# Performance work log

Measured on AMD Instinct MI355X. Metric: run time of the kernel, lower is better.

Reference implementation:

```python
import jax, jax.numpy as jnp
import numpy as np

B, N, I, H, O, E, HD = 4, 2048, 32, 64, 32, 2, 2  # batch, nodes, in_dim, hidden, out, edgetypes, heads
D1 = H * HD * E  # layer-1 filter input dim (concat of all heads/edgetypes from layer 0)


def setup_inputs() -> dict:
    key = jax.random.key(0)
    ks = jax.random.split(key, 20)
    s = 0.1
    return {
        "nodes": jax.random.normal(ks[0], (B, N, I), jnp.float32),
        "edges": jax.random.normal(ks[1], (B, N, N, E), jnp.float32),
        "W_emb": jax.random.normal(ks[2], (I, H), jnp.float32) * s,
        "b_emb": jnp.zeros((H,), jnp.float32),
        "Wf0": jax.random.normal(ks[3], (E, HD, H, H), jnp.float32) * s,
        "w1_0": jax.random.normal(ks[4], (E, HD, H), jnp.float32) * s,
        "b1_0": jnp.zeros((E, HD), jnp.float32),
        "w2_0": jax.random.normal(ks[5], (E, HD, H), jnp.float32) * s,
        "b2_0": jnp.zeros((E, HD), jnp.float32),
        "bias0": jax.random.normal(ks[6], (HD, H), jnp.float32) * s,  # state_bias aliased across edgetypes (list-mult bug)
        "Wf1": jax.random.normal(ks[7], (E, HD, D1, H), jnp.float32) * s,
        "w1_1": jax.random.normal(ks[8], (E, HD, H), jnp.float32) * s,
        "b1_1": jnp.zeros((E, HD), jnp.float32),
        "w2_1": jax.random.normal(ks[9], (E, HD, H), jnp.float32) * s,
        "b2_1": jnp.zeros((E, HD), jnp.float32),
        "bias1": jax.random.normal(ks[10], (HD, H), jnp.float32) * s,
        "W_out": jax.random.normal(ks[11], (H, O), jnp.float32) * s,
        "b_out": jnp.zeros((O,), jnp.float32),
    }


def _gat_layer(state, Wf, w1, b1, w2, b2, bias, edges_t, last):
    # state: (B,N,Din); Wf: (E,HD,Din,H); edges_t: (E,B,N,N)
    Wh = jnp.einsum('bnd,ehdk->ehbnk', state, Wf)                     # (E,HD,B,N,H)
    a1 = jnp.einsum('ehbnk,ehk->ehbn', Wh, w1) + b1[:, :, None, None]
    a2 = jnp.einsum('ehbnk,ehk->ehbn', Wh, w2) + b2[:, :, None, None]
    logits = jax.nn.leaky_relu(a1[..., :, None] + a2[..., None, :], 0.2) + edges_t[:, None]
    att = jax.nn.softmax(logits, axis=-2)                             # torch softmax dim=1 (over rows)
    msg = jnp.einsum('ehbik,ehbkd->ehbid', att, Wh) + bias[None, :, None, None, :]
    if last:
        return jnp.mean(jax.nn.elu(msg), axis=(0, 1))                 # (B,N,H)
    # concat in (edgetype-major, head-minor) order, matching the python loops
    return jnp.transpose(msg, (2, 3, 0, 1, 4)).reshape(msg.shape[2], msg.shape[3], -1)


def reference(nodes, edges, W_emb, b_emb, Wf0, w1_0, b1_0, w2_0, b2_0, bias0,
              Wf1, w1_1, b1_1, w2_1, b2_1, bias1, W_out, b_out):
    edges_t = jnp.transpose(edges, (3, 0, 1, 2))                      # (E,B,N,N)
    state = nodes @ W_emb + b_emb                                     # embedding
    state = _gat_layer(state, Wf0, w1_0, b1_0, w2_0, b2_0, bias0, edges_t, last=False)
    state = _gat_layer(state, Wf1, w1_1, b1_1, w2_1, b2_1, bias1, edges_t, last=True)
    out = state @ W_out + b_out                                       # (B,N,O)
    return jnp.mean(out, axis=1)                                      # graph-level output (B,O)
```

## Files before the change

### kernel.cpp

```cpp
#include <hip/hip_runtime.h>
#include <hip/hip_bf16.h>


constexpr int B_  = 4;
constexpr int N_  = 2048;
constexpr int I_  = 32;
constexpr int H_  = 64;
constexpr int O_  = 32;
constexpr int EH_ = 4;
constexpr int D1_ = 256;
constexpr int BN_ = B_ * N_;
constexpr int NC_ = 64;
constexpr int CH_ = N_ / NC_;
constexpr int TI_ = 16;
constexpr int TK_ = 32;
constexpr int NKT_ = N_ / TK_;

typedef __bf16 bf16x8 __attribute__((ext_vector_type(8)));
typedef float floatx4 __attribute__((ext_vector_type(4)));

constexpr float L2E_ = 1.4426950408889634f;

__device__ __forceinline__ unsigned short f2b(float f) {
    unsigned int u = __float_as_uint(f);
    return (unsigned short)((u + 0x7fffu + ((u >> 16) & 1u)) >> 16);
}

__device__ __forceinline__ float fexp2(float x) {
#if __has_builtin(__builtin_amdgcn_exp2f)
    return __builtin_amdgcn_exp2f(x);
#else
    return __expf(x * 0.6931471805599453f);
#endif
}

__global__ __launch_bounds__(256) void prep_kernel(
        const float* __restrict__ nodes, const float* __restrict__ W_emb,
        const float* __restrict__ b_emb, const float* __restrict__ Wf0,
        const float* __restrict__ Wf1, unsigned short* __restrict__ state0B,
        unsigned short* __restrict__ WfB0, unsigned short* __restrict__ WfB1) {
    int blk = blockIdx.x;
    int t = threadIdx.x;
    __shared__ float sn[4][I_];
    if (blk < 2048) {
        int r = t >> 6, h = t & 63;
        if (t < 4 * I_) {
            int rr = t / I_, ii = t % I_;
            sn[rr][ii] = nodes[(size_t)(blk * 4 + rr) * I_ + ii];
        }
        __syncthreads();
        float acc = b_emb[h];
        #pragma unroll
        for (int i = 0; i < I_; ++i) acc += sn[r][i] * W_emb[i * H_ + h];
        state0B[(size_t)(blk * 4 + r) * H_ + h] = f2b(acc);
    } else if (blk < 2048 + 64) {
        int o = (blk - 2048) * 256 + t;
        int k = o & 63, n = (o >> 6) & 63, c = o >> 12;
        WfB0[o] = f2b(Wf0[((size_t)c * 64 + k) * 64 + n]);
    } else {
        int o = (blk - 2112) * 256 + t;
        int k = o & 255, n = (o >> 8) & 63, c = o >> 14;
        WfB1[o] = f2b(Wf1[((size_t)c * 256 + k) * 64 + n]);
    }
}

template <int DIN>
__global__ __launch_bounds__(256) void wh_a_mfma_kernel(
        const unsigned short* __restrict__ stateB, const unsigned short* __restrict__ WfB,
        const float* __restrict__ w1, const float* __restrict__ b1,
        const float* __restrict__ w2, const float* __restrict__ b2,
        unsigned short* __restrict__ WhB, float* __restrict__ a1,
        float* __restrict__ a2) {
    int t = threadIdx.x;
    int lane = t & 63, wv = t >> 6;
    int col = lane & 15, qd = lane >> 4;
    int bn0 = blockIdx.x * TI_;
    int b = bn0 >> 11;

    floatx4 acc[4] = {{0,0,0,0},{0,0,0,0},{0,0,0,0},{0,0,0,0}};
    const unsigned short* __restrict__ ap = stateB + (size_t)(bn0 + col) * DIN + qd * 8;
    const unsigned short* __restrict__ bp = WfB + ((size_t)(wv * 64 + col) * DIN + qd * 8);
    #pragma unroll
    for (int k0 = 0; k0 < DIN; k0 += 32) {
        bf16x8 af = *(const bf16x8*)(ap + k0);
        #pragma unroll
        for (int nt = 0; nt < 4; ++nt) {
            bf16x8 bf = *(const bf16x8*)(bp + (size_t)nt * 16 * DIN + k0);
            acc[nt] = __builtin_amdgcn_mfma_f32_16x16x32_bf16(af, bf, acc[nt], 0, 0, 0);
        }
    }
    int nb = ((bn0 & 2047) >> 3) + (qd >> 1);
    #pragma unroll
    for (int nt = 0; nt < 4; ++nt) {
        unsigned int lo = (unsigned int)f2b(acc[nt][0]) | ((unsigned int)f2b(acc[nt][1]) << 16);
        unsigned int hi = (unsigned int)f2b(acc[nt][2]) | ((unsigned int)f2b(acc[nt][3]) << 16);
        uint2 v = make_uint2(lo, hi);
        *(uint2*)(WhB + ((((size_t)(wv * B_ + b) * 256 + nb) * 64 + nt * 16 + col) * 8
                         + (qd & 1) * 4)) = v;
    }
    float p1[4] = {}, p2[4] = {};
    #pragma unroll
    for (int nt = 0; nt < 4; ++nt) {
        float w1n = w1[wv * H_ + nt * 16 + col];
        float w2n = w2[wv * H_ + nt * 16 + col];
        #pragma unroll
        for (int r = 0; r < 4; ++r) {
            p1[r] += acc[nt][r] * w1n;
            p2[r] += acc[nt][r] * w2n;
        }
    }
    #pragma unroll
    for (int m = 1; m < 16; m <<= 1)
        #pragma unroll
        for (int r = 0; r < 4; ++r) {
            p1[r] += __shfl_xor(p1[r], m, 64);
            p2[r] += __shfl_xor(p2[r], m, 64);
        }
    if (col == 0) {
        float b1c = b1[wv], b2c = b2[wv];
        #pragma unroll
        for (int r = 0; r < 4; ++r) {
            a1[(size_t)wv * BN_ + bn0 + qd * 4 + r] = (p1[r] + b1c) * L2E_;
            a2[(size_t)wv * BN_ + bn0 + qd * 4 + r] = (p2[r] + b2c) * L2E_;
        }
    }
}

__global__ __launch_bounds__(256) void stats_kernel(
        const float* __restrict__ edges, const float* __restrict__ a1,
        const float* __restrict__ a2, float* __restrict__ ps) {
    int blk = blockIdx.x;
    int jt = blk & 3;
    int ic = (blk >> 2) & (NC_ - 1);
    int b  = blk >> 8;
    int t = threadIdx.x;
    int j0 = jt * 512 + t * 2;
    __shared__ float sa1[EH_][CH_];
    if (t < EH_ * CH_) {
        int cc = t >> 5, ii = t & 31;
        sa1[cc][ii] = a1[(size_t)cc * BN_ + b * N_ + ic * CH_ + ii];
    }
    __syncthreads();
    float a2x[EH_], a2y[EH_], s0[EH_], s1[EH_];
    #pragma unroll
    for (int cc = 0; cc < EH_; ++cc) {
        float2 av = *(const float2*)(a2 + (size_t)cc * BN_ + b * N_ + j0);
        a2x[cc] = av.x; a2y[cc] = av.y;
        s0[cc] = 0.f; s1[cc] = 0.f;
    }
    const float4* __restrict__ ep =
        (const float4*)edges + (((size_t)(b * N_ + ic * CH_) * N_ + j0) >> 1);
    #pragma unroll 4
    for (int ii = 0; ii < CH_; ++ii) {
        float4 u = ep[(size_t)ii * (N_ >> 1)];
        #pragma unroll
        for (int cc = 0; cc < EH_; ++cc) {
            float base = sa1[cc][ii];
            float xa = base + a2x[cc];
            float xb = base + a2y[cc];
            float la = fmaxf(xa, 0.2f * xa);
            float lb = fmaxf(xb, 0.2f * xb);
            float ea = (cc < 2) ? u.x : u.y;
            float eb = (cc < 2) ? u.z : u.w;
            s0[cc] += fexp2(fmaf(ea, L2E_, la));
            s1[cc] += fexp2(fmaf(eb, L2E_, lb));
        }
    }
    #pragma unroll
    for (int cc = 0; cc < EH_; ++cc)
        *(float2*)&ps[((size_t)ic * EH_ + cc) * BN_ + b * N_ + j0] =
            make_float2(s0[cc], s1[cc]);
}

__global__ __launch_bounds__(256) void scale_kernel(
        const float* __restrict__ ps, unsigned short* __restrict__ WhB) {
    int t = threadIdx.x;
    int m0 = blockIdx.x * 256;
    int cb = m0 >> 14;
    int c = cb >> 2, b = cb & 3;
    int k0 = ((m0 >> 6) & 255) * 8;
    __shared__ float sD[32];
    if (t < 32) {
        float S = 0.f;
        const float* pp = ps + (size_t)c * BN_ + b * N_ + k0 + t;
        #pragma unroll 8
        for (int ic = 0; ic < NC_; ++ic) S += pp[(size_t)ic * EH_ * BN_];
        sD[t] = 1.f / S;
    }
    __syncthreads();
    unsigned short* wp = WhB + (size_t)(m0 + t) * 8;
    uint4 w = *(const uint4*)wp;
    int nbo = (t >> 6) * 8;
    unsigned int words[4] = {w.x, w.y, w.z, w.w};
    #pragma unroll
    for (int q = 0; q < 4; ++q) {
        float lo = __uint_as_float((words[q] & 0xffffu) << 16) * sD[nbo + 2 * q];
        float hi = __uint_as_float(words[q] & 0xffff0000u) * sD[nbo + 2 * q + 1];
        words[q] = (unsigned)f2b(lo) | ((unsigned)f2b(hi) << 16);
    }
    *(uint4*)wp = make_uint4(words[0], words[1], words[2], words[3]);
}

template <int LAST>
__global__ __launch_bounds__(512, 8) void mac_kernel(
        const float* __restrict__ edges, const float* __restrict__ a1,
        const float* __restrict__ a2s, const unsigned short* __restrict__ WhB,
        const float* __restrict__ bias, void* __restrict__ outv) {
    int t = threadIdx.x;
    int blk = blockIdx.x;
    int cp = blk & 1;
    int g  = blk >> 1;
    int b  = g >> 7;
    int i0 = (g & 127) * TI_;
    int lane = t & 63, wv = t >> 6;
    int kq = wv >> 1;
    int cl = wv & 1;
    int c  = cp * 2 + cl;
    int col = lane & 15;
    int qd  = lane >> 4;

    __shared__ float sa2[2][N_];
    __shared__ float sA[2][TI_][H_ + 1];
    __shared__ float sB[2][TI_][H_ + 1];

    for (int q = t; q < 2 * (N_ / 4); q += 512) {
        int cl_ = q >> 9, kk = q & 511;
        ((float4*)sa2[cl_])[kk] =
            ((const float4*)(a2s + (size_t)(cp * 2 + cl_) * BN_ + b * N_))[kk];
    }

    float a1v = a1[(size_t)c * BN_ + b * N_ + i0 + col];
    const float* __restrict__ erow = edges + (size_t)(b * N_ + i0 + col) * (N_ * 2);
    const unsigned short* __restrict__ whb0 = WhB + (size_t)(c * B_ + b) * (N_ * 64);

    floatx4 acc[4] = {{0,0,0,0},{0,0,0,0},{0,0,0,0},{0,0,0,0}};
    __syncthreads();

    const int ktBeg = kq * (NKT_ / 4);
    const int ktEnd = ktBeg + NKT_ / 4;
    for (int kt = ktBeg; kt < ktEnd; ++kt) {
        const float4* ep = (const float4*)(erow + (size_t)(kt * TK_ + qd * 8) * 2);
        float4 e0 = ep[0], e1 = ep[1], e2 = ep[2], e3 = ep[3];
        bf16x8 bf[4];
        #pragma unroll
        for (int nt = 0; nt < 4; ++nt)
            bf[nt] = *(const bf16x8*)(whb0 + ((size_t)(kt * 4 + qd) * 64 + nt * 16 + col) * 8);
        const float4* sp = (const float4*)&sa2[cl][kt * TK_ + qd * 8];
        float4 s0 = sp[0], s1 = sp[1];
        float az[8] = {s0.x, s0.y, s0.z, s0.w, s1.x, s1.y, s1.z, s1.w};
        float ev[8];
        ev[0] = cp ? e0.y : e0.x; ev[1] = cp ? e0.w : e0.z;
        ev[2] = cp ? e1.y : e1.x; ev[3] = cp ? e1.w : e1.z;
        ev[4] = cp ? e2.y : e2.x; ev[5] = cp ? e2.w : e2.z;
        ev[6] = cp ? e3.y : e3.x; ev[7] = cp ? e3.w : e3.z;
        bf16x8 af;
        #pragma unroll
        for (int j = 0; j < 8; ++j) {
            float sx = a1v + az[j];
            float u  = fmaxf(sx, 0.2f * sx);
            af[j] = (__bf16)fexp2(fmaf(ev[j], L2E_, u));
        }
        #pragma unroll
        for (int nt = 0; nt < 4; ++nt)
            acc[nt] = __builtin_amdgcn_mfma_f32_16x16x32_bf16(af, bf[nt], acc[nt], 0, 0, 0);
    }

    if (kq == 2) {
        #pragma unroll
        for (int nt = 0; nt < 4; ++nt)
            #pragma unroll
            for (int r = 0; r < 4; ++r)
                sA[cl][qd * 4 + r][nt * 16 + col] = acc[nt][r];
    } else if (kq == 3) {
        #pragma unroll
        for (int nt = 0; nt < 4; ++nt)
            #pragma unroll
            for (int r = 0; r < 4; ++r)
                sB[cl][qd * 4 + r][nt * 16 + col] = acc[nt][r];
    }
    __syncthreads();
    if (kq == 0) {
        #pragma unroll
        for (int nt = 0; nt < 4; ++nt)
            #pragma unroll
            for (int r = 0; r < 4; ++r)
                acc[nt][r] += sA[cl][qd * 4 + r][nt * 16 + col];
    } else if (kq == 1) {
        #pragma unroll
        for (int nt = 0; nt < 4; ++nt)
            #pragma unroll
            for (int r = 0; r < 4; ++r)
                acc[nt][r] += sB[cl][qd * 4 + r][nt * 16 + col];
    }
    __syncthreads();
    if (kq == 1) {
        #pragma unroll
        for (int nt = 0; nt < 4; ++nt)
            #pragma unroll
            for (int r = 0; r < 4; ++r)
                sA[cl][qd * 4 + r][nt * 16 + col] = acc[nt][r];
    }
    __syncthreads();
    if (kq == 0) {
        if (LAST) {
            #pragma unroll
            for (int nt = 0; nt < 4; ++nt) {
                float bb = bias[cl * H_ + nt * 16 + col];
                #pragma unroll
                for (int r = 0; r < 4; ++r) {
                    float x = acc[nt][r] + sA[cl][qd * 4 + r][nt * 16 + col] + bb;
                    sA[cl][qd * 4 + r][nt * 16 + col] =
                        x > 0.f ? x : (__expf(x) - 1.f);
                }
            }
        } else {
            unsigned short* out = (unsigned short*)outv;
            #pragma unroll
            for (int nt = 0; nt < 4; ++nt) {
                float bb = bias[cl * H_ + nt * 16 + col];
                #pragma unroll
                for (int r = 0; r < 4; ++r) {
                    float x = acc[nt][r] + sA[cl][qd * 4 + r][nt * 16 + col] + bb;
                    out[((size_t)(b * N_ + i0 + qd * 4 + r)) * D1_ + c * H_ + nt * 16 + col]
                        = f2b(x);
                }
            }
        }
    }
    if (LAST) {
        __syncthreads();
        if (t < 64) {
            float s = 0.f;
            #pragma unroll
            for (int r = 0; r < TI_; ++r)
                s += sA[0][r][t] + sA[1][r][t];
            ((float*)outv)[((size_t)cp * 512 + g) * 64 + t] = s * 0.25f;
        }
    }
}

__global__ __launch_bounds__(1024) void out_kernel(
        const float* __restrict__ po, const float* __restrict__ W_out,
        const float* __restrict__ b_out, float* __restrict__ out) {
    int b = blockIdx.x, t = threadIdx.x;
    int d = t & 63, g0 = t >> 6;
    float s = 0.f;
    #pragma unroll 4
    for (int p = g0; p < 256; p += 16) {
        int cp = p >> 7, it = p & 127;
        s += po[((size_t)cp * 512 + b * 128 + it) * 64 + d];
    }
    __shared__ float red[16][H_];
    red[g0][d] = s;
    __syncthreads();
    if (t < H_) {
        float r = 0.f;
        #pragma unroll
        for (int q = 0; q < 16; ++q) r += red[q][t];
        red[0][t] = r * (1.f / N_);
    }
    __syncthreads();
    if (t < O_) {
        float acc = b_out[t];
        #pragma unroll 8
        for (int dd = 0; dd < H_; ++dd)
            acc += red[0][dd] * W_out[dd * O_ + t];
        out[b * O_ + t] = acc;
    }
}

extern "C" void kernel_launch(void* const* d_in, const int* in_sizes, int n_in,
                              void* d_out, int out_size, void* d_ws, size_t ws_size,
                              hipStream_t stream) {
    const float* nodes = (const float*)d_in[0];
    const float* edges = (const float*)d_in[1];
    const float* W_emb = (const float*)d_in[2];
    const float* b_emb = (const float*)d_in[3];
    const float* Wf0   = (const float*)d_in[4];
    const float* w1_0  = (const float*)d_in[5];
    const float* b1_0  = (const float*)d_in[6];
    const float* w2_0  = (const float*)d_in[7];
    const float* b2_0  = (const float*)d_in[8];
    const float* bias0 = (const float*)d_in[9];
    const float* Wf1   = (const float*)d_in[10];
    const float* w1_1  = (const float*)d_in[11];
    const float* b1_1  = (const float*)d_in[12];
    const float* w2_1  = (const float*)d_in[13];
    const float* b2_1  = (const float*)d_in[14];
    const float* bias1 = (const float*)d_in[15];
    const float* W_out = (const float*)d_in[16];
    const float* b_out = (const float*)d_in[17];

    float* ws = (float*)d_ws;
    unsigned short* state0B = (unsigned short*)ws;
    unsigned short* state1B = (unsigned short*)(ws + 262144);
    unsigned short* WhB  = (unsigned short*)(ws + 262144 + 1048576);
    unsigned short* WfB0 = (unsigned short*)(ws + 2359296);
    unsigned short* WfB1 = (unsigned short*)(ws + 2367488);
    float* a1 = ws + 2400256;
    float* a2 = ws + 2433024;
    float* ps = ws + 2465792;
    float* po = ws + 4562944;

    prep_kernel<<<2368, 256, 0, stream>>>(nodes, W_emb, b_emb, Wf0, Wf1,
                                          state0B, WfB0, WfB1);

    wh_a_mfma_kernel<H_><<<BN_ / TI_, 256, 0, stream>>>(state0B, WfB0, w1_0, b1_0,
                                                        w2_0, b2_0, WhB, a1, a2);
    stats_kernel<<<B_ * NC_ * (N_ / 512), 256, 0, stream>>>(edges, a1, a2, ps);
    scale_kernel<<<1024, 256, 0, stream>>>(ps, WhB);
    mac_kernel<0><<<2 * B_ * (N_ / TI_), 512, 0, stream>>>(edges, a1, a2, WhB, bias0, state1B);
    wh_a_mfma_kernel<D1_><<<BN_ / TI_, 256, 0, stream>>>(state1B, WfB1, w1_1, b1_1,
                                                         w2_1, b2_1, WhB, a1, a2);
    stats_kernel<<<B_ * NC_ * (N_ / 512), 256, 0, stream>>>(edges, a1, a2, ps);
    scale_kernel<<<1024, 256, 0, stream>>>(ps, WhB);
    mac_kernel<1><<<2 * B_ * (N_ / TI_), 512, 0, stream>>>(edges, a1, a2, WhB, bias1, po);

    out_kernel<<<B_, 1024, 0, stream>>>(po, W_out, b_out, (float*)d_out);
}
```

Measured before the change: 442.2 us.

## Stage edge tiles into LDS with async double-buffered loads in mac kernel

The mac kernel now copies swizzled edge tiles from global memory straight into LDS through global_load_lds, double-buffering them so the next tile loads while the current one is consumed. Before, each lane read edges with strided global loads. Block indices are remapped, probably for cache locality, and the cross-wave reduction is collapsed into a single LDS stage. Stats now uses 128 row chunks, and the scale kernel sums the partials in parallel, which enlarges the partial-sum buffer and moves po. The changes add LDS use (48KB) and a barrier every k-step, which may reduce occupancy.

```diff
diff --git a/kernel.cpp b/kernel.cpp
--- a/kernel.cpp
+++ b/kernel.cpp
@@ -10,11 +10,11 @@
 constexpr int EH_ = 4;
 constexpr int D1_ = 256;
 constexpr int BN_ = B_ * N_;
-constexpr int NC_ = 64;
+constexpr int NC_ = 128;
 constexpr int CH_ = N_ / NC_;
 constexpr int TI_ = 16;
 constexpr int TK_ = 32;
-constexpr int NKT_ = N_ / TK_;
+constexpr int NQT_ = 16;
 
 typedef __bf16 bf16x8 __attribute__((ext_vector_type(8)));
 typedef float floatx4 __attribute__((ext_vector_type(4)));
@@ -32,6 +32,12 @@
 #else
     return __expf(x * 0.6931471805599453f);
 #endif
+}
+
+__device__ __forceinline__ void gl2lds16(const void* g, void* l) {
+    __builtin_amdgcn_global_load_lds(
+        (const __attribute__((address_space(1))) unsigned int*)g,
+        (__attribute__((address_space(3))) unsigned int*)l, 16, 0, 0);
 }
 
 __global__ __launch_bounds__(256) void prep_kernel(
@@ -132,12 +138,12 @@
     int blk = blockIdx.x;
     int jt = blk & 3;
     int ic = (blk >> 2) & (NC_ - 1);
-    int b  = blk >> 8;
+    int b  = blk >> 9;
     int t = threadIdx.x;
     int j0 = jt * 512 + t * 2;
     __shared__ float sa1[EH_][CH_];
     if (t < EH_ * CH_) {
-        int cc = t >> 5, ii = t & 31;
+        int cc = t >> 4, ii = t & 15;
         sa1[cc][ii] = a1[(size_t)cc * BN_ + b * N_ + ic * CH_ + ii];
     }
     __syncthreads();
@@ -179,12 +185,21 @@
     int cb = m0 >> 14;
     int c = cb >> 2, b = cb & 3;
     int k0 = ((m0 >> 6) & 255) * 8;
+    __shared__ float sP[8][32];
     __shared__ float sD[32];
+    {
+        int kk = t & 31, grp = t >> 5;
+        float S = 0.f;
+        const float* pp = ps + (size_t)c * BN_ + b * N_ + k0 + kk
+                        + (size_t)grp * (NC_ / 8) * EH_ * BN_;
+        #pragma unroll 4
+        for (int ic = 0; ic < NC_ / 8; ++ic) S += pp[(size_t)ic * EH_ * BN_];
+        sP[grp][kk] = S;
+    }
+    __syncthreads();
     if (t < 32) {
-        float S = 0.f;
-        const float* pp = ps + (size_t)c * BN_ + b * N_ + k0 + t;
-        #pragma unroll 8
-        for (int ic = 0; ic < NC_; ++ic) S += pp[(size_t)ic * EH_ * BN_];
+        float S = sP[0][t] + sP[1][t] + sP[2][t] + sP[3][t]
+                + sP[4][t] + sP[5][t] + sP[6][t] + sP[7][t];
         sD[t] = 1.f / S;
     }
     __syncthreads();
@@ -202,14 +217,15 @@
 }
 
 template <int LAST>
-__global__ __launch_bounds__(512, 8) void mac_kernel(
+__global__ __launch_bounds__(512, 6) void mac_kernel(
         const float* __restrict__ edges, const float* __restrict__ a1,
         const float* __restrict__ a2s, const unsigned short* __restrict__ WhB,
         const float* __restrict__ bias, void* __restrict__ outv) {
     int t = threadIdx.x;
-    int blk = blockIdx.x;
-    int cp = blk & 1;
-    int g  = blk >> 1;
+    int blk0 = blockIdx.x;
+    int x = blk0 & 7, j = blk0 >> 3;
+    int g  = x * 64 + (j >> 1);
+    int cp = j & 1;
     int b  = g >> 7;
     int i0 = (g & 127) * TI_;
     int lane = t & 63, wv = t >> 6;
@@ -219,9 +235,9 @@
     int col = lane & 15;
     int qd  = lane >> 4;
 
-    __shared__ float sa2[2][N_];
-    __shared__ float sA[2][TI_][H_ + 1];
-    __shared__ float sB[2][TI_][H_ + 1];
+    __shared__ __attribute__((aligned(16))) unsigned char smem[49152];
+    float (*sa2)[N_] = (float(*)[N_])smem;
+    unsigned char* eds = smem + 16384;
 
     for (int q = t; q < 2 * (N_ / 4); q += 512) {
         int cl_ = q >> 9, kk = q & 511;
@@ -230,75 +246,70 @@
     }
 
     float a1v = a1[(size_t)c * BN_ + b * N_ + i0 + col];
-    const float* __restrict__ erow = edges + (size_t)(b * N_ + i0 + col) * (N_ * 2);
     const unsigned short* __restrict__ whb0 = WhB + (size_t)(c * B_ + b) * (N_ * 64);
 
+    int rowA = 8 * cl + (lane >> 4);
+    int rowB = rowA + 4;
+    const char* gr = (const char*)edges;
+    size_t baseA = (size_t)(b * N_ + i0 + rowA) * N_ * 8
+                 + (size_t)((lane & 15) ^ (rowA & 15)) * 16;
+    size_t baseB = (size_t)(b * N_ + i0 + rowB) * N_ * 8
+                 + (size_t)((lane & 15) ^ (rowB & 15)) * 16;
+    unsigned char* ldA = eds + kq * 4096 + (8 * cl) * 256;
+    unsigned char* ldB = ldA + 4 * 256;
+
     floatx4 acc[4] = {{0,0,0,0},{0,0,0,0},{0,0,0,0},{0,0,0,0}};
-    __syncthreads();
-
-    const int ktBeg = kq * (NKT_ / 4);
-    const int ktEnd = ktBeg + NKT_ / 4;
-    for (int kt = ktBeg; kt < ktEnd; ++kt) {
-        const float4* ep = (const float4*)(erow + (size_t)(kt * TK_ + qd * 8) * 2);
-        float4 e0 = ep[0], e1 = ep[1], e2 = ep[2], e3 = ep[3];
+
+    {
+        size_t ko = (size_t)(kq * NQT_) * 256;
+        gl2lds16(gr + baseA + ko, ldA);
+        gl2lds16(gr + baseB + ko, ldB);
+    }
+    for (int s = 0; s < NQT_; ++s) {
+        __syncthreads();
+        if (s + 1 < NQT_) {
+            int buf = (s + 1) & 1;
+            size_t ko = (size_t)(kq * NQT_ + s + 1) * 256;
+            gl2lds16(gr + baseA + ko, ldA + buf * 16384);
+            gl2lds16(gr + baseB + ko, ldB + buf * 16384);
+        }
+        int kt = kq * NQT_ + s;
+        const unsigned char* ebase = eds + (s & 1) * 16384 + kq * 4096 + col * 256;
+        float ev[8];
+        #pragma unroll
+        for (int jj = 0; jj < 4; ++jj) {
+            int sg = qd * 4 + jj;
+            float4 v = *(const float4*)(ebase + (sg ^ col) * 16);
+            ev[2 * jj]     = cp ? v.y : v.x;
+            ev[2 * jj + 1] = cp ? v.w : v.z;
+        }
+        const float4* sp = (const float4*)&sa2[cl][kt * TK_ + qd * 8];
+        float4 z0 = sp[0], z1 = sp[1];
+        float az[8] = {z0.x, z0.y, z0.z, z0.w, z1.x, z1.y, z1.z, z1.w};
         bf16x8 bf[4];
         #pragma unroll
         for (int nt = 0; nt < 4; ++nt)
             bf[nt] = *(const bf16x8*)(whb0 + ((size_t)(kt * 4 + qd) * 64 + nt * 16 + col) * 8);
-        const float4* sp = (const float4*)&sa2[cl][kt * TK_ + qd * 8];
-        float4 s0 = sp[0], s1 = sp[1];
-        float az[8] = {s0.x, s0.y, s0.z, s0.w, s1.x, s1.y, s1.z, s1.w};
-        float ev[8];
-        ev[0] = cp ? e0.y : e0.x; ev[1] = cp ? e0.w : e0.z;
-        ev[2] = cp ? e1.y : e1.x; ev[3] = cp ? e1.w : e1.z;
-        ev[4] = cp ? e2.y : e2.x; ev[5] = cp ? e2.w : e2.z;
-        ev[6] = cp ? e3.y : e3.x; ev[7] = cp ? e3.w : e3.z;
         bf16x8 af;
         #pragma unroll
-        for (int j = 0; j < 8; ++j) {
-            float sx = a1v + az[j];
+        for (int jv = 0; jv < 8; ++jv) {
+            float sx = a1v + az[jv];
             float u  = fmaxf(sx, 0.2f * sx);
-            af[j] = (__bf16)fexp2(fmaf(ev[j], L2E_, u));
+            af[jv] = (__bf16)fexp2(fmaf(ev[jv], L2E_, u));
         }
         #pragma unroll
         for (int nt = 0; nt < 4; ++nt)
             acc[nt] = __builtin_amdgcn_mfma_f32_16x16x32_bf16(af, bf[nt], acc[nt], 0, 0, 0);
     }
 
-    if (kq == 2) {
+    __syncthreads();
+    float (*sred)[2][TI_][H_ + 1] = (float(*)[2][TI_][H_ + 1])smem;
+    if (kq > 0) {
         #pragma unroll
         for (int nt = 0; nt < 4; ++nt)
             #pragma unroll
             for (int r = 0; r < 4; ++r)
-                sA[cl][qd * 4 + r][nt * 16 + col] = acc[nt][r];
-    } else if (kq == 3) {
-        #pragma unroll
-        for (int nt = 0; nt < 4; ++nt)
-            #pragma unroll
-            for (int r = 0; r < 4; ++r)
-                sB[cl][qd * 4 + r][nt * 16 + col] = acc[nt][r];
-    }
-    __syncthreads();
-    if (kq == 0) {
-        #pragma unroll
-        for (int nt = 0; nt < 4; ++nt)
-            #pragma unroll
-            for (int r = 0; r < 4; ++r)
-                acc[nt][r] += sA[cl][qd * 4 + r][nt * 16 + col];
-    } else if (kq == 1) {
-        #pragma unroll
-        for (int nt = 0; nt < 4; ++nt)
-            #pragma unroll
-            for (int r = 0; r < 4; ++r)
-                acc[nt][r] += sB[cl][qd * 4 + r][nt * 16 + col];
-    }
-    __syncthreads();
-    if (kq == 1) {
-        #pragma unroll
-        for (int nt = 0; nt < 4; ++nt)
-            #pragma unroll
-            for (int r = 0; r < 4; ++r)
-                sA[cl][qd * 4 + r][nt * 16 + col] = acc[nt][r];
+                sred[kq - 1][cl][qd * 4 + r][nt * 16 + col] = acc[nt][r];
     }
     __syncthreads();
     if (kq == 0) {
@@ -308,9 +319,12 @@
                 float bb = bias[cl * H_ + nt * 16 + col];
                 #pragma unroll
                 for (int r = 0; r < 4; ++r) {
-                    float x = acc[nt][r] + sA[cl][qd * 4 + r][nt * 16 + col] + bb;
-                    sA[cl][qd * 4 + r][nt * 16 + col] =
-                        x > 0.f ? x : (__expf(x) - 1.f);
+                    float xv = acc[nt][r] + bb
+                             + sred[0][cl][qd * 4 + r][nt * 16 + col]
+                             + sred[1][cl][qd * 4 + r][nt * 16 + col]
+                             + sred[2][cl][qd * 4 + r][nt * 16 + col];
+                    sred[0][cl][qd * 4 + r][nt * 16 + col] =
+                        xv > 0.f ? xv : (__expf(xv) - 1.f);
                 }
             }
         } else {
@@ -320,9 +334,12 @@
                 float bb = bias[cl * H_ + nt * 16 + col];
                 #pragma unroll
                 for (int r = 0; r < 4; ++r) {
-                    float x = acc[nt][r] + sA[cl][qd * 4 + r][nt * 16 + col] + bb;
+                    float xv = acc[nt][r] + bb
+                             + sred[0][cl][qd * 4 + r][nt * 16 + col]
+                             + sred[1][cl][qd * 4 + r][nt * 16 + col]
+                             + sred[2][cl][qd * 4 + r][nt * 16 + col];
                     out[((size_t)(b * N_ + i0 + qd * 4 + r)) * D1_ + c * H_ + nt * 16 + col]
-                        = f2b(x);
+                        = f2b(xv);
                 }
             }
         }
@@ -333,7 +350,7 @@
             float s = 0.f;
             #pragma unroll
             for (int r = 0; r < TI_; ++r)
-                s += sA[0][r][t] + sA[1][r][t];
+                s += sred[0][0][r][t] + sred[0][1][r][t];
             ((float*)outv)[((size_t)cp * 512 + g) * 64 + t] = s * 0.25f;
         }
     }
@@ -400,7 +417,7 @@
     float* a1 = ws + 2400256;
     float* a2 = ws + 2433024;
     float* ps = ws + 2465792;
-    float* po = ws + 4562944;
+    float* po = ws + 6660096;
 
     prep_kernel<<<2368, 256, 0, stream>>>(nodes, W_emb, b_emb, Wf0, Wf1,
                                           state0B, WfB0, WfB1);
```

Measured after the change: 377.2 us. 14.7% less time.
